# Kernel optimization log

Measured on AMD Instinct MI355X. Metric: run time of the kernel, lower is better.

Reference implementation:

```python
import jax, jax.numpy as jnp
import numpy as np

TOTAL_DIM = 64  # 16+16+16+8+8
HIDDEN = 4 * TOTAL_DIM
NUM_HEADS = 8


def _fourier(x, num_freqs):
    # Dyadic Fourier features: sin/cos of 2^j * x for j in [0, num_freqs).
    # Output dim = input_dim * num_freqs * 2 (matches embed_dim in the module).
    freqs = 2.0 ** jnp.arange(num_freqs, dtype=x.dtype)  # (F,)
    phase = x[..., :, None] * freqs                       # (..., in, F)
    out = jnp.concatenate([jnp.sin(phase), jnp.cos(phase)], axis=-1)  # (..., in, 2F)
    return out.reshape(x.shape[:-1] + (-1,))


def setup_inputs() -> dict:
    key = jax.random.key(0)
    k1, k2, k3, k4, k5, k6 = jax.random.split(key, 6)
    B, Nq, Nk, D = 8, 256, 256, 10
    query_states = jax.random.normal(k1, (B, Nq, D), dtype=jnp.float32)
    key_states = jax.random.normal(k2, (B, Nk, D), dtype=jnp.float32)
    W1 = jax.random.normal(k3, (TOTAL_DIM, HIDDEN), dtype=jnp.float32) / np.sqrt(TOTAL_DIM)
    b1 = jnp.zeros((HIDDEN,), dtype=jnp.float32)
    W2 = jax.random.normal(k4, (HIDDEN, NUM_HEADS), dtype=jnp.float32) / np.sqrt(HIDDEN)
    b2 = jnp.zeros((NUM_HEADS,), dtype=jnp.float32)
    return {"query_states": query_states, "key_states": key_states,
            "W1": W1, "b1": b1, "W2": W2, "b2": b2}


def _features(query_states, key_states):
    # Slice per-ship fields, then broadcast pairwise: q -> (B,Nq,1,*), k -> (B,1,Nk,*)
    q_team = query_states[:, :, None, 0]          # (B,Nq,1)
    k_team = key_states[:, None, :, 0]            # (B,1,Nk)
    q_pos = query_states[:, :, None, 3:5]
    k_pos = key_states[:, None, :, 3:5]
    q_vel = query_states[:, :, None, 5:7]
    k_vel = key_states[:, None, :, 5:7]
    q_att = query_states[:, :, None, 7:9]
    k_att = key_states[:, None, :, 7:9]

    delta_pos = k_pos - q_pos                     # (B,Nq,Nk,2)
    delta_vel = k_vel - q_vel                     # (B,Nq,Nk,2)
    feat_delta_input = jnp.concatenate([delta_pos, delta_vel], axis=-1)  # (B,Nq,Nk,4)

    dist_sq = jnp.sum(delta_pos ** 2, axis=-1, keepdims=True)
    dist = jnp.sqrt(dist_sq + 1e-6)
    inv_dist = 1.0 / (dist + 0.1)
    feat_dist_input = jnp.concatenate([dist, inv_dist], axis=-1)         # (B,Nq,Nk,2)

    bearing = delta_pos / (dist + 1e-6)
    ata = jnp.sum(bearing * q_att, axis=-1, keepdims=True)
    aspect = jnp.sum(bearing * k_att, axis=-1, keepdims=True)
    feat_angle_input = jnp.concatenate([ata, aspect], axis=-1)           # (B,Nq,Nk,2)

    dot_dp_dv = jnp.sum(delta_pos * delta_vel, axis=-1, keepdims=True)
    speed_sq = jnp.sum(delta_vel ** 2, axis=-1, keepdims=True)
    ttca = jnp.tanh(jax.nn.relu(-dot_dp_dv / (speed_sq + 1e-6)))
    feat_intercept_input = jnp.concatenate([ttca, dist], axis=-1)        # (B,Nq,Nk,2)

    same_team = (q_team == k_team).astype(query_states.dtype)[..., None]
    q_speed = jnp.linalg.norm(q_vel, axis=-1, keepdims=True)
    k_speed = jnp.linalg.norm(k_vel, axis=-1, keepdims=True)
    delta_speed = k_speed - q_speed
    feat_team_input = jnp.concatenate([same_team, delta_speed], axis=-1)  # (B,Nq,Nk,2)

    out_dist = _fourier(feat_dist_input, 4)        # 16
    out_angle = _fourier(feat_angle_input, 4)      # 16
    out_delta = _fourier(feat_delta_input, 2)      # 16
    out_intercept = _fourier(feat_intercept_input, 2)  # 8
    out_team = _fourier(feat_team_input, 2)        # 8
    return jnp.concatenate([out_dist, out_angle, out_delta, out_intercept, out_team], axis=-1)


def reference(query_states, key_states, W1, b1, W2, b2):
    combined = _features(query_states, key_states)          # (B,Nq,Nk,64)
    h = jax.nn.silu(combined @ W1 + b1)                     # (B,Nq,Nk,256)
    bias = h @ W2 + b2                                      # (B,Nq,Nk,H)
    return jnp.transpose(bias, (0, 3, 1, 2))                # (B,H,Nq,Nk)
```

## Files before the change

kernel.cpp:

```cpp
#include <hip/hip_runtime.h>
#include <math.h>

#define NB 8
#define NQ 256
#define NK 256
#define DIN 10
#define FDIM 64
#define HIDDEN 256
#define NH 8
#define ROWS_PER_BLK 4

#define FSTRIDE 64
#define HSTRIDE 264

typedef float f32x4 __attribute__((ext_vector_type(4)));
typedef float f32x2 __attribute__((ext_vector_type(2)));
typedef short bf16x8 __attribute__((ext_vector_type(8)));

__device__ __forceinline__ short f2bf(float f) {
    return (short)((__float_as_uint(f) + 0x8000u) >> 16);
}
__device__ __forceinline__ unsigned cvtpk(float a, float b) {
    unsigned r;
    asm("v_cvt_pk_bf16_f32 %0, %1, %2" : "=v"(r) : "v"(a), "v"(b));
    return r;
}
__device__ __forceinline__ float rcpf(float x) { return __builtin_amdgcn_rcpf(x); }
__device__ __forceinline__ float ex2f(float x) { return __builtin_amdgcn_exp2f(x); }
__device__ __forceinline__ float sqtf(float x) { return __builtin_amdgcn_sqrtf(x); }

__device__ __forceinline__ void four4(float x, float* dst) {
    float s1 = __sinf(x), c1 = __cosf(x);
    float s2 = 2.f * s1 * c1, c2 = 1.f - 2.f * s1 * s1;
    float s4 = 2.f * s2 * c2, c4 = 1.f - 2.f * s2 * s2;
    float s8 = 2.f * s4 * c4, c8 = 1.f - 2.f * s4 * s4;
    dst[0] = s1; dst[1] = s2; dst[2] = s4; dst[3] = s8;
    dst[4] = c1; dst[5] = c2; dst[6] = c4; dst[7] = c8;
}
__device__ __forceinline__ void four2(float x, float* dst) {
    float s1 = __sinf(x), c1 = __cosf(x);
    dst[0] = s1; dst[1] = 2.f * s1 * c1;
    dst[2] = c1; dst[3] = 1.f - 2.f * s1 * s1;
}

__global__ __attribute__((amdgpu_flat_work_group_size(512, 512),
                          amdgpu_waves_per_eu(4, 4)))
void relfeat_mfma_kernel(
    const float* __restrict__ q, const float* __restrict__ k,
    const float* __restrict__ W1, const float* __restrict__ b1,
    const float* __restrict__ W2, const float* __restrict__ b2,
    float* __restrict__ out)
{
    __shared__ __align__(16) short feat_s[NK * FSTRIDE];
    __shared__ __align__(16) short h_s[64 * HSTRIDE];

    const int t = threadIdx.x;
    const int wave = t >> 6;
    const int lane15 = t & 15;
    const int quad = (t >> 4) & 3;
    const int p = t & 255;
    const int b = blockIdx.x >> 6;
    const int i0 = (blockIdx.x & 63) * ROWS_PER_BLK;

    const float* kp = k + ((size_t)b * NK + p) * DIN;
    const float k0 = kp[0], k3 = kp[3], k4 = kp[4], k5 = kp[5], k6 = kp[6],
                k7 = kp[7], k8 = kp[8];
    const float k_speed = sqtf(k5 * k5 + k6 * k6);

    bf16x8 w2f[8];
    if (wave < 4) {
#pragma unroll
        for (int ks = 0; ks < 8; ++ks) {
            const float* wp = W2 + (size_t)(ks * 32 + quad * 8) * NH + (lane15 & 7);
            bf16x8 v;
#pragma unroll
            for (int e = 0; e < 8; ++e)
                v[e] = f2bf(-0.69314718f * wp[(size_t)e * NH]);
            w2f[ks] = v;
        }
    }

    const int n0 = wave * 32;
    bf16x8 w1f[2][2];
#pragma unroll
    for (int nt = 0; nt < 2; ++nt)
#pragma unroll
        for (int ks = 0; ks < 2; ++ks) {
            const float* wp = W1 + (size_t)(ks * 32 + quad * 8) * HIDDEN
                              + (n0 + nt * 16 + lane15);
            bf16x8 v;
#pragma unroll
            for (int e = 0; e < 8; ++e)
                v[e] = f2bf(-1.44269504f * wp[(size_t)e * HIDDEN]);
            w1f[nt][ks] = v;
        }
    f32x4 b1c[2];
#pragma unroll
    for (int nt = 0; nt < 2; ++nt) {
        float4 bb = *(const float4*)&b1[n0 + nt * 16 + quad * 4];
        b1c[nt] = (f32x4){-1.44269504f * bb.x, -1.44269504f * bb.y,
                          -1.44269504f * bb.z, -1.44269504f * bb.w};
    }
    const float b2v = (lane15 < NH) ? b2[lane15] : 0.f;
    float* const outp = out + ((size_t)b * NH + (lane15 & 7)) * NQ * NK
                        + wave * 16 + quad * 4;

    const int sw = p & 7;
    const int swr = lane15 & 7;
    const f32x2 one2 = {1.f, 1.f};

    auto fstore = [&](int c8, const float* f8) {
        uint4 v;
        v.x = cvtpk(f8[0], f8[1]);
        v.y = cvtpk(f8[2], f8[3]);
        v.z = cvtpk(f8[4], f8[5]);
        v.w = cvtpk(f8[6], f8[7]);
        *(uint4*)&feat_s[p * FSTRIDE + ((c8 ^ sw) * 8)] = v;
    };
    auto feat_full = [&](int irow) {
        const float* qp = q + ((size_t)b * NQ + irow) * DIN;
        const float q0 = qp[0], q3 = qp[3], q4 = qp[4], q5 = qp[5],
                    q6 = qp[6], q7 = qp[7], q8 = qp[8];
        const float dpx = k3 - q3, dpy = k4 - q4;
        const float dvx = k5 - q5, dvy = k6 - q6;
        const float dist = sqtf(dpx * dpx + dpy * dpy + 1e-6f);
        float f8[8];
        four4(dist, f8);
        const float ds1 = f8[0], ds2 = f8[1], dc1 = f8[4], dc2 = f8[5];
        fstore(0, f8);
        four4(rcpf(dist + 0.1f), f8);
        fstore(1, f8);
        {
            const float inv_d2 = rcpf(dist + 1e-6f);
            const float bx = dpx * inv_d2, by = dpy * inv_d2;
            four4(bx * q7 + by * q8, f8); fstore(2, f8);
            four4(bx * k7 + by * k8, f8); fstore(3, f8);
        }
        four2(dpx, f8); four2(dpy, f8 + 4); fstore(4, f8);
        four2(dvx, f8); four2(dvy, f8 + 4); fstore(5, f8);
        {
            const float dd = dpx * dvx + dpy * dvy;
            const float ss = dvx * dvx + dvy * dvy;
            const float z = fmaxf(0.f, -dd * rcpf(ss + 1e-6f));
            const float ttca = 1.f - 2.f * rcpf(1.f + ex2f(2.88539008f * z));
            four2(ttca, f8);
            f8[4] = ds1; f8[5] = ds2; f8[6] = dc1; f8[7] = dc2;
            fstore(6, f8);
        }
        {
            const bool st = (q0 == k0);
            f8[0] = st ? 0.84147098f : 0.f;
            f8[1] = st ? 0.90929743f : 0.f;
            f8[2] = st ? 0.54030231f : 1.f;
            f8[3] = st ? -0.41614684f : 1.f;
            const float qs = sqtf(q5 * q5 + q6 * q6);
            four2(k_speed - qs, f8 + 4);
            fstore(7, f8);
        }
    };

    if (wave >= 4)
        feat_full(i0);
    __syncthreads();

#pragma unroll 1
    for (int row = 0; row < ROWS_PER_BLK; ++row) {
        const int i = i0 + row;

#pragma unroll 1
        for (int c = 0; c < 4; ++c) {
            const int p0 = c * 64;

            f32x4 acc[2][4];
#pragma unroll
            for (int mt = 0; mt < 4; ++mt) {
                const int r2 = p0 + mt * 16 + lane15;
                const bf16x8 fb = *(const bf16x8*)
                    &feat_s[r2 * FSTRIDE + ((quad ^ swr) * 8)];
                acc[0][mt] = __builtin_amdgcn_mfma_f32_16x16x32_bf16(
                    w1f[0][0], fb, b1c[0], 0, 0, 0);
                acc[1][mt] = __builtin_amdgcn_mfma_f32_16x16x32_bf16(
                    w1f[1][0], fb, b1c[1], 0, 0, 0);
            }
#pragma unroll
            for (int mt = 0; mt < 4; ++mt) {
                const int r2 = p0 + mt * 16 + lane15;
                const bf16x8 fb = *(const bf16x8*)
                    &feat_s[r2 * FSTRIDE + (((4 + quad) ^ swr) * 8)];
#pragma unroll
                for (int nt = 0; nt < 2; ++nt)
                    acc[nt][mt] = __builtin_amdgcn_mfma_f32_16x16x32_bf16(
                        w1f[nt][1], fb, acc[nt][mt], 0, 0, 0);
            }

            uint2 pk[2][4];
#pragma unroll
            for (int nt = 0; nt < 2; ++nt)
#pragma unroll
                for (int mt = 0; mt < 4; ++mt) {
                    const f32x4 a = acc[nt][mt];
                    const f32x2 a01 = {a[0], a[1]}, a23 = {a[2], a[3]};
                    const f32x2 e01 = {ex2f(a[0]), ex2f(a[1])};
                    const f32x2 e23 = {ex2f(a[2]), ex2f(a[3])};
                    const f32x2 t01 = e01 + one2;
                    const f32x2 t23 = e23 + one2;
                    const f32x2 r01 = {rcpf(t01[0]), rcpf(t01[1])};
                    const f32x2 r23 = {rcpf(t23[0]), rcpf(t23[1])};
                    const f32x2 s01 = a01 * r01;
                    const f32x2 s23 = a23 * r23;
                    pk[nt][mt].x = cvtpk(s01[0], s01[1]);
                    pk[nt][mt].y = cvtpk(s23[0], s23[1]);
                }

            __syncthreads();

#pragma unroll
            for (int nt = 0; nt < 2; ++nt)
#pragma unroll
                for (int mt = 0; mt < 4; ++mt) {
                    const int pair = mt * 16 + lane15;
                    const int hbase = n0 + nt * 16 + quad * 4;
                    *(uint2*)&h_s[pair * HSTRIDE + hbase] = pk[nt][mt];
                }
            __syncthreads();

            if (wave < 4) {
                const int pw = wave * 16;
                f32x4 acc2 = (f32x4){b2v, b2v, b2v, b2v};
#pragma unroll
                for (int ks = 0; ks < 8; ++ks) {
                    const bf16x8 ha = *(const bf16x8*)&h_s[(pw + lane15) * HSTRIDE
                                                            + ks * 32 + quad * 8];
                    acc2 = __builtin_amdgcn_mfma_f32_16x16x32_bf16(ha, w2f[ks], acc2, 0, 0, 0);
                }
                if (lane15 < NH) {
                    float* op = outp + (size_t)i * NK + p0;
                    *(float4*)op = make_float4(acc2[0], acc2[1], acc2[2], acc2[3]);
                }
            } else if (c == 3 && row + 1 < ROWS_PER_BLK) {
                feat_full(i + 1);
            }
        }

        if (row + 1 < ROWS_PER_BLK)
            __syncthreads();
    }
}

extern "C" void kernel_launch(void* const* d_in, const int* in_sizes, int n_in,
                              void* d_out, int out_size, void* d_ws, size_t ws_size,
                              hipStream_t stream) {
    const float* q  = (const float*)d_in[0];
    const float* k  = (const float*)d_in[1];
    const float* W1 = (const float*)d_in[2];
    const float* b1 = (const float*)d_in[3];
    const float* W2 = (const float*)d_in[4];
    const float* b2 = (const float*)d_in[5];
    float* out = (float*)d_out;

    dim3 grid(NB * NQ / ROWS_PER_BLK);
    dim3 block(512);
    relfeat_mfma_kernel<<<grid, block, 0, stream>>>(q, k, W1, b1, W2, b2, out);
}
```

Measured before the change: 108.2 us.

## Double-buffer per-chunk feature tiles and spread feature work across all waves

Replaces the full-row feature buffer with a two-slot 64-pair buffer. The next chunk's features are computed by the two waves (one per half of the block) that own that pair range, with each half producing a different subset of the features, and this happens between the MLP stages instead of being done by the upper four waves at row end. This removes the per-row extra barrier and the serialized feature pass, and shrinks LDS use. Rows per block drop to 2, doubling the grid, and the waves-per-EU hint is raised to allow higher occupancy, at the risk of register spills and more repeated per-block W1/W2 setup.

```diff
diff --git a/kernel.cpp b/kernel.cpp
--- a/kernel.cpp
+++ b/kernel.cpp
@@ -8,7 +8,7 @@
 #define FDIM 64
 #define HIDDEN 256
 #define NH 8
-#define ROWS_PER_BLK 4
+#define ROWS_PER_BLK 2
 
 #define FSTRIDE 64
 #define HSTRIDE 264
@@ -44,14 +44,14 @@
 }
 
 __global__ __attribute__((amdgpu_flat_work_group_size(512, 512),
-                          amdgpu_waves_per_eu(4, 4)))
+                          amdgpu_waves_per_eu(6, 8)))
 void relfeat_mfma_kernel(
     const float* __restrict__ q, const float* __restrict__ k,
     const float* __restrict__ W1, const float* __restrict__ b1,
     const float* __restrict__ W2, const float* __restrict__ b2,
     float* __restrict__ out)
 {
-    __shared__ __align__(16) short feat_s[NK * FSTRIDE];
+    __shared__ __align__(16) short feat2[2][64 * FSTRIDE];
     __shared__ __align__(16) short h_s[64 * HSTRIDE];
 
     const int t = threadIdx.x;
@@ -59,8 +59,9 @@
     const int lane15 = t & 15;
     const int quad = (t >> 4) & 3;
     const int p = t & 255;
-    const int b = blockIdx.x >> 6;
-    const int i0 = (blockIdx.x & 63) * ROWS_PER_BLK;
+    const int half = t >> 8;
+    const int b = blockIdx.x >> 7;
+    const int i0 = (blockIdx.x & 127) * ROWS_PER_BLK;
 
     const float* kp = k + ((size_t)b * NK + p) * DIN;
     const float k0 = kp[0], k3 = kp[3], k4 = kp[4], k5 = kp[5], k6 = kp[6],
@@ -107,17 +108,10 @@
 
     const int sw = p & 7;
     const int swr = lane15 & 7;
+    const int lp = p & 63;
     const f32x2 one2 = {1.f, 1.f};
 
-    auto fstore = [&](int c8, const float* f8) {
-        uint4 v;
-        v.x = cvtpk(f8[0], f8[1]);
-        v.y = cvtpk(f8[2], f8[3]);
-        v.z = cvtpk(f8[4], f8[5]);
-        v.w = cvtpk(f8[6], f8[7]);
-        *(uint4*)&feat_s[p * FSTRIDE + ((c8 ^ sw) * 8)] = v;
-    };
-    auto feat_full = [&](int irow) {
+    auto feat_task = [&](int irow, int wbuf) {
         const float* qp = q + ((size_t)b * NQ + irow) * DIN;
         const float q0 = qp[0], q3 = qp[3], q4 = qp[4], q5 = qp[5],
                     q6 = qp[6], q7 = qp[7], q8 = qp[8];
@@ -125,42 +119,46 @@
         const float dvx = k5 - q5, dvy = k6 - q6;
         const float dist = sqtf(dpx * dpx + dpy * dpy + 1e-6f);
         float f8[8];
-        four4(dist, f8);
-        const float ds1 = f8[0], ds2 = f8[1], dc1 = f8[4], dc2 = f8[5];
-        fstore(0, f8);
-        four4(rcpf(dist + 0.1f), f8);
-        fstore(1, f8);
-        {
-            const float inv_d2 = rcpf(dist + 1e-6f);
-            const float bx = dpx * inv_d2, by = dpy * inv_d2;
-            four4(bx * q7 + by * q8, f8); fstore(2, f8);
-            four4(bx * k7 + by * k8, f8); fstore(3, f8);
-        }
-        four2(dpx, f8); four2(dpy, f8 + 4); fstore(4, f8);
-        four2(dvx, f8); four2(dvy, f8 + 4); fstore(5, f8);
-        {
+        auto fstore = [&](int c8) {
+            uint4 v;
+            v.x = cvtpk(f8[0], f8[1]);
+            v.y = cvtpk(f8[2], f8[3]);
+            v.z = cvtpk(f8[4], f8[5]);
+            v.w = cvtpk(f8[6], f8[7]);
+            *(uint4*)&feat2[wbuf][lp * FSTRIDE + ((c8 ^ sw) * 8)] = v;
+        };
+        if (half == 0) {
+            four4(dist, f8);
+            const float ds1 = f8[0], ds2 = f8[1], dc1 = f8[4], dc2 = f8[5];
+            fstore(0);
+            four4(rcpf(dist + 0.1f), f8);
+            fstore(1);
             const float dd = dpx * dvx + dpy * dvy;
             const float ss = dvx * dvx + dvy * dvy;
             const float z = fmaxf(0.f, -dd * rcpf(ss + 1e-6f));
             const float ttca = 1.f - 2.f * rcpf(1.f + ex2f(2.88539008f * z));
             four2(ttca, f8);
             f8[4] = ds1; f8[5] = ds2; f8[6] = dc1; f8[7] = dc2;
-            fstore(6, f8);
-        }
-        {
+            fstore(6);
             const bool st = (q0 == k0);
             f8[0] = st ? 0.84147098f : 0.f;
             f8[1] = st ? 0.90929743f : 0.f;
             f8[2] = st ? 0.54030231f : 1.f;
             f8[3] = st ? -0.41614684f : 1.f;
-            const float qs = sqtf(q5 * q5 + q6 * q6);
-            four2(k_speed - qs, f8 + 4);
-            fstore(7, f8);
+            four2(k_speed - sqtf(q5 * q5 + q6 * q6), f8 + 4);
+            fstore(7);
+        } else {
+            const float inv_d2 = rcpf(dist + 1e-6f);
+            const float bx = dpx * inv_d2, by = dpy * inv_d2;
+            four4(bx * q7 + by * q8, f8); fstore(2);
+            four4(bx * k7 + by * k8, f8); fstore(3);
+            four2(dpx, f8); four2(dpy, f8 + 4); fstore(4);
+            four2(dvx, f8); four2(dvy, f8 + 4); fstore(5);
         }
     };
 
-    if (wave >= 4)
-        feat_full(i0);
+    if ((p >> 6) == 0)
+        feat_task(i0, 0);
     __syncthreads();
 
 #pragma unroll 1
@@ -170,13 +168,14 @@
 #pragma unroll 1
         for (int c = 0; c < 4; ++c) {
             const int p0 = c * 64;
+            const int rb = c & 1;
 
             f32x4 acc[2][4];
 #pragma unroll
             for (int mt = 0; mt < 4; ++mt) {
-                const int r2 = p0 + mt * 16 + lane15;
+                const int lp2 = mt * 16 + lane15;
                 const bf16x8 fb = *(const bf16x8*)
-                    &feat_s[r2 * FSTRIDE + ((quad ^ swr) * 8)];
+                    &feat2[rb][lp2 * FSTRIDE + ((quad ^ swr) * 8)];
                 acc[0][mt] = __builtin_amdgcn_mfma_f32_16x16x32_bf16(
                     w1f[0][0], fb, b1c[0], 0, 0, 0);
                 acc[1][mt] = __builtin_amdgcn_mfma_f32_16x16x32_bf16(
@@ -184,9 +183,9 @@
             }
 #pragma unroll
             for (int mt = 0; mt < 4; ++mt) {
-                const int r2 = p0 + mt * 16 + lane15;
+                const int lp2 = mt * 16 + lane15;
                 const bf16x8 fb = *(const bf16x8*)
-                    &feat_s[r2 * FSTRIDE + (((4 + quad) ^ swr) * 8)];
+                    &feat2[rb][lp2 * FSTRIDE + (((4 + quad) ^ swr) * 8)];
 #pragma unroll
                 for (int nt = 0; nt < 2; ++nt)
                     acc[nt][mt] = __builtin_amdgcn_mfma_f32_16x16x32_bf16(
@@ -212,6 +211,13 @@
                     pk[nt][mt].y = cvtpk(s23[0], s23[1]);
                 }
 
+            {
+                const int tc = (c + 1) & 3;
+                const bool last = (row == ROWS_PER_BLK - 1) && (c == 3);
+                if ((p >> 6) == tc && !last)
+                    feat_task(i + (c == 3), (c + 1) & 1);
+            }
+
             __syncthreads();
 
 #pragma unroll
@@ -237,13 +243,8 @@
                     float* op = outp + (size_t)i * NK + p0;
                     *(float4*)op = make_float4(acc2[0], acc2[1], acc2[2], acc2[3]);
                 }
-            } else if (c == 3 && row + 1 < ROWS_PER_BLK) {
-                feat_full(i + 1);
-            }
-        }
-
-        if (row + 1 < ROWS_PER_BLK)
-            __syncthreads();
+            }
+        }
     }
 }
 
```

Measured after the change: 149.0 us. +37.6%, slower.
